# Kernel optimization log

Hardware: AMD Instinct MI355X
Metric: run time of the kernel (lower is better)

## Reference

```python
import jax, jax.numpy as jnp
import numpy as np

EMBED_DIM = 512
NUM_HEADS = 8
HEAD_DIM = EMBED_DIM // NUM_HEADS
PAIR_BONUS = 2.0
MIN_SEPARATION = 3
PAIRING_MATRIX = jnp.array([
    [0, 1, 0, 0, 0],
    [1, 0, 1, 0, 0],
    [0, 1, 0, 1, 0],
    [0, 0, 1, 0, 0],
    [0, 0, 0, 0, 0],
], dtype=jnp.float32)


def setup_inputs() -> dict:
    key = jax.random.key(0)
    ks = jax.random.split(key, 12)
    B, S, E = 8, 1024, EMBED_DIM
    scale = 1.0 / np.sqrt(E)
    inp = {
        "query": jax.random.normal(ks[0], (B, S, E), dtype=jnp.float32),
        "key": jax.random.normal(ks[1], (B, S, E), dtype=jnp.float32),
        "value": jax.random.normal(ks[2], (B, S, E), dtype=jnp.float32),
        "nucleotide_sequence": jax.random.randint(ks[3], (B, S), 0, 5, dtype=jnp.int32),
        "key_padding_mask": jnp.zeros((B, S), dtype=bool),
        "Wq": jax.random.normal(ks[4], (E, E), dtype=jnp.float32) * scale,
        "bq": jnp.zeros((E,), dtype=jnp.float32),
        "Wk": jax.random.normal(ks[5], (E, E), dtype=jnp.float32) * scale,
        "bk": jnp.zeros((E,), dtype=jnp.float32),
        "Wv": jax.random.normal(ks[6], (E, E), dtype=jnp.float32) * scale,
        "bv": jnp.zeros((E,), dtype=jnp.float32),
        "Wo": jax.random.normal(ks[7], (E, E), dtype=jnp.float32) * scale,
        "bo": jnp.zeros((E,), dtype=jnp.float32),
    }
    return inp


def reference(query, key, value, nucleotide_sequence, key_padding_mask,
              Wq, bq, Wk, bk, Wv, bv, Wo, bo):
    B, T, E = query.shape
    S = key.shape[1]
    H, D = NUM_HEADS, HEAD_DIM
    scaling = D ** -0.5

    # projections -> (B, H, L, D)
    q = (query @ Wq + bq).reshape(B, T, H, D).transpose(0, 2, 1, 3)
    k = (key @ Wk + bk).reshape(B, S, H, D).transpose(0, 2, 1, 3)
    v = (value @ Wv + bv).reshape(B, S, H, D).transpose(0, 2, 1, 3)

    attn = jnp.einsum('bhtd,bhsd->bhts', q, k) * scaling  # (B,H,T,S)

    # base-pairing bias: gather into 5x5 table, masked by min separation
    pos = jnp.arange(S)
    sep_ok = (jnp.abs(pos[:, None] - pos[None, :]) >= MIN_SEPARATION).astype(jnp.float32)
    pairing = PAIRING_MATRIX[nucleotide_sequence[:, :, None], nucleotide_sequence[:, None, :]]  # (B,S,S)
    pair_bonus = pairing * sep_ok[None] * PAIR_BONUS
    attn = attn + pair_bonus[:, None, :, :]

    # key padding mask -> -inf
    attn = jnp.where(key_padding_mask[:, None, None, :], -jnp.inf, attn)

    attn_probs = jax.nn.softmax(attn, axis=-1)
    out = jnp.einsum('bhts,bhsd->bhtd', attn_probs, v)
    out = out.transpose(0, 2, 1, 3).reshape(B, T, E)
    out = out @ Wo + bo
    return out, attn_probs
```

## Files before the change

### kernel.cpp

```cpp
#include <hip/hip_runtime.h>
#include <hip/hip_bf16.h>
#include <stdint.h>


typedef float  f32x4  __attribute__((ext_vector_type(4)));
typedef short  s16x8  __attribute__((ext_vector_type(8)));

__device__ __forceinline__ ushort f2bf(float f) {
  union { float f; uint32_t u; } v; v.f = f;
  uint32_t u = v.u;
  return (ushort)((u + 0x7FFF + ((u >> 16) & 1)) >> 16);
}

__device__ __forceinline__ float bf2f(uint32_t u) {
  union { uint32_t u; float f; } v; v.u = u << 16;
  return v.f;
}

__device__ __forceinline__ f32x4 mfma16(s16x8 a, s16x8 b, f32x4 c) {
  return __builtin_amdgcn_mfma_f32_16x16x32_bf16(a, b, c, 0, 0, 0);
}

__device__ __forceinline__ void gl_lds16(const void* g, void* l) {
  typedef __attribute__((address_space(1))) const void gvoid;
  typedef __attribute__((address_space(3))) void lvoid;
  __builtin_amdgcn_global_load_lds((gvoid*)(uintptr_t)g,
                                   (lvoid*)(uint32_t)(uintptr_t)l, 16, 0, 0);
}

__device__ __forceinline__ void vwait4() {
  asm volatile("s_waitcnt vmcnt(4)" ::: "memory");
  __builtin_amdgcn_sched_barrier(0);
}
__device__ __forceinline__ void vwait0() {
  asm volatile("s_waitcnt vmcnt(0)" ::: "memory");
  __builtin_amdgcn_sched_barrier(0);
}
__device__ __forceinline__ void bar_lds() {
  asm volatile("s_waitcnt lgkmcnt(0)" ::: "memory");
  __builtin_amdgcn_s_barrier();
  __builtin_amdgcn_sched_barrier(0);
}

__global__ __launch_bounds__(256) void k_convert_w(
    const float* __restrict__ Wq, const float* __restrict__ Wk,
    const float* __restrict__ Wv, const float* __restrict__ Wo,
    ushort* __restrict__ WT, ushort* __restrict__ WoT) {
  int idx = blockIdx.x * 256 + threadIdx.x;
  int row = idx >> 9;
  int k = idx & 511;
  if (row < 1536) {
    const float* W = (row < 512) ? Wq : (row < 1024 ? Wk : Wv);
    int n = row & 511;
    WT[row * 512 + k] = f2bf(W[k * 512 + n]);
  } else {
    int n = row - 1536;
    WoT[n * 512 + k] = f2bf(Wo[k * 512 + n]);
  }
}

__global__ __launch_bounds__(256) void k_gemm_qkv(
    const float* __restrict__ Aq, const float* __restrict__ Ak,
    const float* __restrict__ Av, const ushort* __restrict__ WT,
    const float* __restrict__ bq, const float* __restrict__ bk,
    const float* __restrict__ bv, ushort* __restrict__ Y) {
  __shared__ ushort As[128 * 64];
  __shared__ ushort Bs[128 * 64];
  const int id = blockIdx.x;
  const int xcd = id & 7, slot = id >> 3;
  const int mb = xcd * 8 + slot / 12;
  const int nb = slot % 12;
  const int mat = nb >> 2;
  const float* A    = (mat == 0) ? Aq : (mat == 1 ? Ak : Av);
  const float* bias = (mat == 0) ? bq : (mat == 1 ? bk : bv);
  const int tid = threadIdx.x;
  const int w = tid >> 6, l = tid & 63;
  const int wr = (w >> 1) * 64, wc = (w & 1) * 64;
  const int lr = l & 15, lg = l >> 4;
  const int srow = l >> 3, sslot = (l & 7) ^ srow;

  f32x4 acc[4][4];
#pragma unroll
  for (int i = 0; i < 4; i++)
#pragma unroll
    for (int j = 0; j < 4; j++) acc[i][j] = (f32x4){0.f, 0.f, 0.f, 0.f};

  for (int kk = 0; kk < 8; kk++) {
    const int k0 = kk * 64;
#pragma unroll
    for (int it = 0; it < 8; it++) {
      int s2 = it * 256 + tid;
      int row = s2 >> 4;
      int k4 = (s2 & 15) * 4;
      float4 v = *reinterpret_cast<const float4*>(
          &A[(size_t)(mb * 128 + row) * 512 + k0 + k4]);
      uint64_t p = (uint64_t)f2bf(v.x) | ((uint64_t)f2bf(v.y) << 16) |
                   ((uint64_t)f2bf(v.z) << 32) | ((uint64_t)f2bf(v.w) << 48);
      int boff = row * 128 + ((k4 * 2) ^ ((row & 7) << 4));
      *reinterpret_cast<uint64_t*>((char*)As + boff) = p;
    }
#pragma unroll
    for (int it = 0; it < 4; it++) {
      int g8 = it * 4 + w;
      int row = g8 * 8 + srow;
      gl_lds16(&WT[(size_t)(nb * 128 + row) * 512 + k0 + sslot * 8], &Bs[g8 * 512]);
    }
    __syncthreads();
#pragma unroll
    for (int ks = 0; ks < 2; ks++) {
      s16x8 af[4], bfr[4];
#pragma unroll
      for (int mt = 0; mt < 4; mt++) {
        int row = wr + mt * 16 + lr;
        af[mt] = *reinterpret_cast<const s16x8*>(
            (char*)As + row * 128 + ((ks * 64 + lg * 16) ^ ((row & 7) << 4)));
      }
#pragma unroll
      for (int nt = 0; nt < 4; nt++) {
        int row = wc + nt * 16 + lr;
        bfr[nt] = *reinterpret_cast<const s16x8*>(
            (char*)Bs + row * 128 + ((ks * 64 + lg * 16) ^ ((row & 7) << 4)));
      }
#pragma unroll
      for (int mt = 0; mt < 4; mt++)
#pragma unroll
        for (int nt = 0; nt < 4; nt++)
          acc[mt][nt] = mfma16(af[mt], bfr[nt], acc[mt][nt]);
    }
    __syncthreads();
  }
  const int ncb = nb * 128;
#pragma unroll
  for (int nt = 0; nt < 4; nt++) {
    int gcol = ncb + wc + nt * 16 + lr;
    float bv_ = bias[gcol & 511];
#pragma unroll
    for (int mt = 0; mt < 4; mt++) {
#pragma unroll
      for (int r = 0; r < 4; r++) {
        int grow = mb * 128 + wr + mt * 16 + lg * 4 + r;
        Y[(size_t)grow * 1536 + gcol] = f2bf(acc[mt][nt][r] + bv_);
      }
    }
  }
}

__global__ __launch_bounds__(256) void k_transpose_v(
    const ushort* __restrict__ Y, ushort* __restrict__ vT) {
  __shared__ ushort T[64 * 64];
  const int sc = blockIdx.x;
  const int bh = blockIdx.y;
  const int b = bh >> 3, h = bh & 7;
  const int s0 = sc * 64;
  const int tid = threadIdx.x;
#pragma unroll
  for (int it = 0; it < 2; it++) {
    int slot = it * 256 + tid;
    int srw = slot >> 3;
    int i16 = (slot & 7) * 16;
    int4 v = *reinterpret_cast<const int4*>(
        &Y[(size_t)(b * 1024 + s0 + srw) * 1536 + 1024 + h * 64 + (slot & 7) * 8]);
    *reinterpret_cast<int4*>((char*)T + srw * 128 + (i16 ^ ((srw & 7) << 4))) = v;
  }
  __syncthreads();
  const int d = tid >> 2;
  const int sseg = (tid & 3) * 16;
  int pk[8];
#pragma unroll
  for (int j = 0; j < 8; j++) {
    int s0l = sseg + 2 * j;
    uint32_t a = *reinterpret_cast<const ushort*>(
        (char*)T + s0l * 128 + ((d * 2) ^ ((s0l & 7) << 4)));
    uint32_t bb = *reinterpret_cast<const ushort*>(
        (char*)T + (s0l + 1) * 128 + ((d * 2) ^ (((s0l + 1) & 7) << 4)));
    pk[j] = (int)(a | (bb << 16));
  }
  ushort* dst = &vT[(size_t)(bh * 64 + d) * 1024 + s0 + sseg];
  int4 o0 = {pk[0], pk[1], pk[2], pk[3]};
  int4 o1 = {pk[4], pk[5], pk[6], pk[7]};
  *reinterpret_cast<int4*>(dst) = o0;
  *reinterpret_cast<int4*>(dst + 8) = o1;
}

__global__ __launch_bounds__(256, 4) void k_attention(
    const ushort* __restrict__ Y, const ushort* __restrict__ vT,
    const int* __restrict__ seq, const unsigned char* __restrict__ mask,
    float* __restrict__ probs, ushort* __restrict__ AO) {
  __shared__ ushort Kb[2][4096];
  __shared__ ushort Vb[2][4096];
  __shared__ ushort Qb[1024];
  __shared__ ushort Pb[16 * 72];
  __shared__ ushort seqm[1024];
  __shared__ float rinv_s[16];
  float* Rbuf = reinterpret_cast<float*>(&Kb[0][0]);

  const int id = blockIdx.x;
  const int xcd = id & 7, slot = id >> 3;
  const int bh = xcd * 8 + (slot >> 6);
  const int tb = slot & 63;
  const int b = bh >> 3, h = bh & 7;
  const int tid = threadIdx.x;
  const int w = tid >> 6, l = tid & 63;
  const int lr = l & 15, lg = l >> 4;
  const int sc_ = w * 16;
  const int srw = sc_ + lr;
  const int srow = l >> 3, sslot = (l & 7) ^ srow;

#pragma unroll
  for (int it = 0; it < 4; it++) {
    int s = it * 256 + tid;
    seqm[s] = (ushort)(seq[b * 1024 + s] | (mask[b * 1024 + s] ? 0x100 : 0));
  }
#pragma unroll
  for (int it = 0; it < 2; it++) {
    int g8 = w * 2 + it;
    int row = g8 * 8 + srow;
    gl_lds16(&Y[(size_t)(b * 1024 + row) * 1536 + 512 + h * 64 + sslot * 8],
             &Kb[0][g8 * 512]);
    gl_lds16(&vT[(size_t)(bh * 64 + row) * 1024 + sslot * 8], &Vb[0][g8 * 512]);
  }
  if (w < 2) {
    gl_lds16(&Y[(size_t)(b * 1024 + tb * 16 + w * 8 + srow) * 1536 + h * 64 +
                sslot * 8],
             &Qb[w * 512]);
  }
  __syncthreads();

  s16x8 qf0 = *reinterpret_cast<const s16x8*>(
      (char*)Qb + lr * 128 + ((lg * 16) ^ ((lr & 7) << 4)));
  s16x8 qf1 = *reinterpret_cast<const s16x8*>(
      (char*)Qb + lr * 128 + ((64 + lg * 16) ^ ((lr & 7) << 4)));
  int seqt[4];
#pragma unroll
  for (int r = 0; r < 4; r++) seqt[r] = seqm[tb * 16 + lg * 4 + r] & 255;

  uint2 pe[16];
  float psum[4] = {0.f, 0.f, 0.f, 0.f};
  f32x4 oacc = (f32x4){0.f, 0.f, 0.f, 0.f};

#pragma unroll
  for (int c = 0; c < 16; c++) {
    if (c < 15) {
#pragma unroll
      for (int it = 0; it < 2; it++) {
        int g8 = w * 2 + it;
        int row = g8 * 8 + srow;
        gl_lds16(&Y[(size_t)(b * 1024 + (c + 1) * 64 + row) * 1536 + 512 +
                    h * 64 + sslot * 8],
                 &Kb[(c + 1) & 1][g8 * 512]);
        gl_lds16(&vT[(size_t)(bh * 64 + row) * 1024 + (c + 1) * 64 + sslot * 8],
                 &Vb[(c + 1) & 1][g8 * 512]);
      }
      vwait4();
    } else {
      vwait0();
    }
    s16x8 kf0 = *reinterpret_cast<const s16x8*>(
        (char*)&Kb[c & 1][0] + srw * 128 + ((lg * 16) ^ ((srw & 7) << 4)));
    s16x8 kf1 = *reinterpret_cast<const s16x8*>(
        (char*)&Kb[c & 1][0] + srw * 128 + ((64 + lg * 16) ^ ((srw & 7) << 4)));
    f32x4 facc = (f32x4){0.f, 0.f, 0.f, 0.f};
    facc = mfma16(qf0, kf0, facc);
    facc = mfma16(qf1, kf1, facc);

    const int sg = c * 64 + srw;
    const int sm = seqm[sg];
    const int ss = sm & 255;
    const bool msk = (sm & 0x100) != 0;
    ushort eb[4];
#pragma unroll
    for (int r = 0; r < 4; r++) {
      int tg = tb * 16 + lg * 4 + r;
      int dsep = tg - sg; dsep = dsep < 0 ? -dsep : dsep;
      int dnt = seqt[r] - ss; dnt = dnt < 0 ? -dnt : dnt;
      bool bon = (dnt == 1 && seqt[r] <= 3 && ss <= 3 && dsep >= 3);
      float v = facc[r] * 0.125f + (bon ? 2.0f : 0.0f);
      float ee = msk ? 0.0f : __expf(v - 12.0f);
      psum[r] += ee;
      eb[r] = f2bf(ee);
      Pb[(lg * 4 + r) * 72 + srw] = eb[r];
    }
    pe[c].x = (uint32_t)eb[0] | ((uint32_t)eb[1] << 16);
    pe[c].y = (uint32_t)eb[2] | ((uint32_t)eb[3] << 16);
    bar_lds();

#pragma unroll
    for (int ks = 0; ks < 2; ks++) {
      s16x8 paf = *reinterpret_cast<const s16x8*>(&Pb[lr * 72 + ks * 32 + lg * 8]);
      s16x8 vb = *reinterpret_cast<const s16x8*>(
          (char*)&Vb[c & 1][0] + srw * 128 +
          ((ks * 64 + lg * 16) ^ ((srw & 7) << 4)));
      oacc = mfma16(paf, vb, oacc);
    }
    bar_lds();
  }

#pragma unroll
  for (int r = 0; r < 4; r++) Rbuf[((w * 4 + lg) * 4 + r) * 16 + lr] = psum[r];
  __syncthreads();
  {
    int row = tid >> 4, j = tid & 15;
    int lgr = row >> 2, rr = row & 3;
    float s = 0.f;
#pragma unroll
    for (int i = 0; i < 4; i++) {
      int wj = j >> 2;
      int lrj = (j & 3) * 4 + i;
      s += Rbuf[((wj * 4 + lgr) * 4 + rr) * 16 + lrj];
    }
#pragma unroll
    for (int off = 1; off < 16; off <<= 1) s += __shfl_xor(s, off);
    if (j == 0) rinv_s[row] = 1.0f / s;
  }
  __syncthreads();
  float rv[4];
#pragma unroll
  for (int r = 0; r < 4; r++) rv[r] = rinv_s[lg * 4 + r];

#pragma unroll
  for (int r = 0; r < 4; r++) {
    int t = tb * 16 + lg * 4 + r;
    AO[((size_t)b * 1024 + t) * 512 + h * 64 + sc_ + lr] = f2bf(oacc[r] * rv[r]);
  }

  float* Pf = reinterpret_cast<float*>(&Kb[0][0]);
  const int prow_ = tid >> 4, pj = tid & 15;
  float* pdst_base = &probs[((size_t)bh * 1024 + tb * 16 + prow_) * 1024 + pj * 4];
#pragma unroll
  for (int c = 0; c < 16; c++) {
#pragma unroll
    for (int r = 0; r < 4; r++) {
      uint32_t u = (r < 2) ? pe[c].x : pe[c].y;
      u = (u >> ((r & 1) * 16)) & 0xffffu;
      Pf[(lg * 4 + r) * 68 + srw] = bf2f(u) * rv[r];
    }
    bar_lds();
    float4 p4 = *reinterpret_cast<const float4*>(&Pf[prow_ * 68 + pj * 4]);
    *reinterpret_cast<float4*>(pdst_base + c * 64) = p4;
    bar_lds();
  }
}

__global__ __launch_bounds__(256) void k_gemm_o(
    const ushort* __restrict__ AO, const ushort* __restrict__ WoT,
    const float* __restrict__ bo, float* __restrict__ out) {
  __shared__ ushort As[128 * 64];
  __shared__ ushort Bs[128 * 64];
  const int id = blockIdx.x;
  const int xcd = id & 7, slot = id >> 3;
  const int mb = xcd * 8 + (slot >> 2);
  const int nb = slot & 3;
  const int tid = threadIdx.x;
  const int w = tid >> 6, l = tid & 63;
  const int wr = (w >> 1) * 64, wc = (w & 1) * 64;
  const int lr = l & 15, lg = l >> 4;
  const int srow = l >> 3, sslot = (l & 7) ^ srow;

  f32x4 acc[4][4];
#pragma unroll
  for (int i = 0; i < 4; i++)
#pragma unroll
    for (int j = 0; j < 4; j++) acc[i][j] = (f32x4){0.f, 0.f, 0.f, 0.f};

  for (int kk = 0; kk < 8; kk++) {
    const int k0 = kk * 64;
#pragma unroll
    for (int it = 0; it < 4; it++) {
      int g8 = it * 4 + w;
      int row = g8 * 8 + srow;
      gl_lds16(&AO[(size_t)(mb * 128 + row) * 512 + k0 + sslot * 8], &As[g8 * 512]);
      gl_lds16(&WoT[(size_t)(nb * 128 + row) * 512 + k0 + sslot * 8], &Bs[g8 * 512]);
    }
    __syncthreads();
#pragma unroll
    for (int ks = 0; ks < 2; ks++) {
      s16x8 af[4], bfr[4];
#pragma unroll
      for (int mt = 0; mt < 4; mt++) {
        int row = wr + mt * 16 + lr;
        af[mt] = *reinterpret_cast<const s16x8*>(
            (char*)As + row * 128 + ((ks * 64 + lg * 16) ^ ((row & 7) << 4)));
      }
#pragma unroll
      for (int nt = 0; nt < 4; nt++) {
        int row = wc + nt * 16 + lr;
        bfr[nt] = *reinterpret_cast<const s16x8*>(
            (char*)Bs + row * 128 + ((ks * 64 + lg * 16) ^ ((row & 7) << 4)));
      }
#pragma unroll
      for (int mt = 0; mt < 4; mt++)
#pragma unroll
        for (int nt = 0; nt < 4; nt++)
          acc[mt][nt] = mfma16(af[mt], bfr[nt], acc[mt][nt]);
    }
    __syncthreads();
  }
  const int ncb = nb * 128;
#pragma unroll
  for (int nt = 0; nt < 4; nt++) {
    int gcol = ncb + wc + nt * 16 + lr;
    float bv_ = bo[gcol];
#pragma unroll
    for (int mt = 0; mt < 4; mt++) {
#pragma unroll
      for (int r = 0; r < 4; r++) {
        int grow = mb * 128 + wr + mt * 16 + lg * 4 + r;
        out[(size_t)grow * 512 + gcol] = acc[mt][nt][r] + bv_;
      }
    }
  }
}

extern "C" void kernel_launch(void* const* d_in, const int* in_sizes, int n_in,
                              void* d_out, int out_size, void* d_ws, size_t ws_size,
                              hipStream_t stream) {
  (void)in_sizes; (void)n_in; (void)out_size; (void)ws_size;
  const float* query = (const float*)d_in[0];
  const float* key   = (const float*)d_in[1];
  const float* value = (const float*)d_in[2];
  const int* seq     = (const int*)d_in[3];
  const unsigned char* mask = (const unsigned char*)d_in[4];
  const float* Wq = (const float*)d_in[5];
  const float* bq = (const float*)d_in[6];
  const float* Wk = (const float*)d_in[7];
  const float* bk = (const float*)d_in[8];
  const float* Wv = (const float*)d_in[9];
  const float* bv = (const float*)d_in[10];
  const float* Wo = (const float*)d_in[11];
  const float* bo = (const float*)d_in[12];

  float* out = (float*)d_out;
  float* probs = out + (size_t)8 * 1024 * 512;

  char* ws = (char*)d_ws;
  ushort* Y   = (ushort*)(ws);
  ushort* WT  = (ushort*)(ws + 25165824);
  ushort* WoT = (ushort*)(ws + 26738688);
  ushort* vT  = (ushort*)(ws + 27262976);
  ushort* AO  = (ushort*)(ws + 35651584);

  k_convert_w<<<4096, 256, 0, stream>>>(Wq, Wk, Wv, Wo, WT, WoT);
  k_gemm_qkv<<<768, 256, 0, stream>>>(query, key, value, WT, bq, bk, bv, Y);
  k_transpose_v<<<dim3(16, 64), 256, 0, stream>>>(Y, vT);
  k_attention<<<4096, 256, 0, stream>>>(Y, vT, seq, mask, probs, AO);
  k_gemm_o<<<256, 256, 0, stream>>>(AO, WoT, bo, out);
}
```

Baseline: 217.1 us.

## Split probability output into separate kernel that recomputes QK scores

```diff
diff --git a/kernel.cpp b/kernel.cpp
--- a/kernel.cpp
+++ b/kernel.cpp
@@ -10,11 +10,6 @@
   union { float f; uint32_t u; } v; v.f = f;
   uint32_t u = v.u;
   return (ushort)((u + 0x7FFF + ((u >> 16) & 1)) >> 16);
-}
-
-__device__ __forceinline__ float bf2f(uint32_t u) {
-  union { uint32_t u; float f; } v; v.u = u << 16;
-  return v.f;
 }
 
 __device__ __forceinline__ f32x4 mfma16(s16x8 a, s16x8 b, f32x4 c) {
@@ -30,6 +25,10 @@
 
 __device__ __forceinline__ void vwait4() {
   asm volatile("s_waitcnt vmcnt(4)" ::: "memory");
+  __builtin_amdgcn_sched_barrier(0);
+}
+__device__ __forceinline__ void vwait2() {
+  asm volatile("s_waitcnt vmcnt(2)" ::: "memory");
   __builtin_amdgcn_sched_barrier(0);
 }
 __device__ __forceinline__ void vwait0() {
@@ -182,10 +181,10 @@
   *reinterpret_cast<int4*>(dst + 8) = o1;
 }
 
-__global__ __launch_bounds__(256, 4) void k_attention(
+__global__ __launch_bounds__(256, 4) void k_attn_core(
     const ushort* __restrict__ Y, const ushort* __restrict__ vT,
     const int* __restrict__ seq, const unsigned char* __restrict__ mask,
-    float* __restrict__ probs, ushort* __restrict__ AO) {
+    float* __restrict__ rinv_ws, ushort* __restrict__ AO) {
   __shared__ ushort Kb[2][4096];
   __shared__ ushort Vb[2][4096];
   __shared__ ushort Qb[1024];
@@ -234,7 +233,6 @@
 #pragma unroll
   for (int r = 0; r < 4; r++) seqt[r] = seqm[tb * 16 + lg * 4 + r] & 255;
 
-  uint2 pe[16];
   float psum[4] = {0.f, 0.f, 0.f, 0.f};
   f32x4 oacc = (f32x4){0.f, 0.f, 0.f, 0.f};
 
@@ -267,7 +265,6 @@
     const int sm = seqm[sg];
     const int ss = sm & 255;
     const bool msk = (sm & 0x100) != 0;
-    ushort eb[4];
 #pragma unroll
     for (int r = 0; r < 4; r++) {
       int tg = tb * 16 + lg * 4 + r;
@@ -277,11 +274,8 @@
       float v = facc[r] * 0.125f + (bon ? 2.0f : 0.0f);
       float ee = msk ? 0.0f : __expf(v - 12.0f);
       psum[r] += ee;
-      eb[r] = f2bf(ee);
-      Pb[(lg * 4 + r) * 72 + srw] = eb[r];
-    }
-    pe[c].x = (uint32_t)eb[0] | ((uint32_t)eb[1] << 16);
-    pe[c].y = (uint32_t)eb[2] | ((uint32_t)eb[3] << 16);
+      Pb[(lg * 4 + r) * 72 + srw] = f2bf(ee);
+    }
     bar_lds();
 
 #pragma unroll
@@ -313,6 +307,8 @@
     if (j == 0) rinv_s[row] = 1.0f / s;
   }
   __syncthreads();
+  if (tid < 16)
+    rinv_ws[(size_t)bh * 1024 + tb * 16 + tid] = rinv_s[tid];
   float rv[4];
 #pragma unroll
   for (int r = 0; r < 4; r++) rv[r] = rinv_s[lg * 4 + r];
@@ -322,22 +318,99 @@
     int t = tb * 16 + lg * 4 + r;
     AO[((size_t)b * 1024 + t) * 512 + h * 64 + sc_ + lr] = f2bf(oacc[r] * rv[r]);
   }
-
-  float* Pf = reinterpret_cast<float*>(&Kb[0][0]);
-  const int prow_ = tid >> 4, pj = tid & 15;
-  float* pdst_base = &probs[((size_t)bh * 1024 + tb * 16 + prow_) * 1024 + pj * 4];
+}
+
+__global__ __launch_bounds__(256, 8) void k_probs(
+    const ushort* __restrict__ Y, const float* __restrict__ rinv_ws,
+    const int* __restrict__ seq, const unsigned char* __restrict__ mask,
+    float* __restrict__ probs) {
+  __shared__ ushort Kb[2][4096];
+  __shared__ ushort Qb[1024];
+  __shared__ unsigned char seqm8[1024];
+
+  const int id = blockIdx.x;
+  const int xcd = id & 7, slot = id >> 3;
+  const int bh = xcd * 8 + (slot >> 6);
+  const int tb = slot & 63;
+  const int b = bh >> 3, h = bh & 7;
+  const int tid = threadIdx.x;
+  const int w = tid >> 6, l = tid & 63;
+  const int lr = l & 15, lg = l >> 4;
+  const int srw = w * 16 + lr;
+  const int srow = l >> 3, sslot = (l & 7) ^ srow;
+
+#pragma unroll
+  for (int it = 0; it < 4; it++) {
+    int s = it * 256 + tid;
+    seqm8[s] =
+        (unsigned char)(seq[b * 1024 + s] | (mask[b * 1024 + s] ? 16 : 0));
+  }
+#pragma unroll
+  for (int it = 0; it < 2; it++) {
+    int g8 = w * 2 + it;
+    int row = g8 * 8 + srow;
+    gl_lds16(&Y[(size_t)(b * 1024 + row) * 1536 + 512 + h * 64 + sslot * 8],
+             &Kb[0][g8 * 512]);
+  }
+  if (w < 2) {
+    gl_lds16(&Y[(size_t)(b * 1024 + tb * 16 + w * 8 + srow) * 1536 + h * 64 +
+                sslot * 8],
+             &Qb[w * 512]);
+  }
+  __syncthreads();
+
+  s16x8 qf0 = *reinterpret_cast<const s16x8*>(
+      (char*)Qb + lr * 128 + ((lg * 16) ^ ((lr & 7) << 4)));
+  s16x8 qf1 = *reinterpret_cast<const s16x8*>(
+      (char*)Qb + lr * 128 + ((64 + lg * 16) ^ ((lr & 7) << 4)));
+  int seqt[4];
+  float rv[4];
+  float* prow[4];
+#pragma unroll
+  for (int r = 0; r < 4; r++) {
+    int t = tb * 16 + lg * 4 + r;
+    seqt[r] = seqm8[t] & 15;
+    rv[r] = rinv_ws[(size_t)bh * 1024 + t];
+    prow[r] = &probs[((size_t)bh * 1024 + t) * 1024 + srw];
+  }
+
 #pragma unroll
   for (int c = 0; c < 16; c++) {
+    if (c < 15) {
+#pragma unroll
+      for (int it = 0; it < 2; it++) {
+        int g8 = w * 2 + it;
+        int row = g8 * 8 + srow;
+        gl_lds16(&Y[(size_t)(b * 1024 + (c + 1) * 64 + row) * 1536 + 512 +
+                    h * 64 + sslot * 8],
+                 &Kb[(c + 1) & 1][g8 * 512]);
+      }
+      vwait2();
+    } else {
+      vwait0();
+    }
+    s16x8 kf0 = *reinterpret_cast<const s16x8*>(
+        (char*)&Kb[c & 1][0] + srw * 128 + ((lg * 16) ^ ((srw & 7) << 4)));
+    s16x8 kf1 = *reinterpret_cast<const s16x8*>(
+        (char*)&Kb[c & 1][0] + srw * 128 + ((64 + lg * 16) ^ ((srw & 7) << 4)));
+    f32x4 facc = (f32x4){0.f, 0.f, 0.f, 0.f};
+    facc = mfma16(qf0, kf0, facc);
+    facc = mfma16(qf1, kf1, facc);
+
+    const int sg = c * 64 + srw;
+    const int sm = seqm8[sg];
+    const int ss = sm & 15;
+    const bool msk = (sm & 16) != 0;
 #pragma unroll
     for (int r = 0; r < 4; r++) {
-      uint32_t u = (r < 2) ? pe[c].x : pe[c].y;
-      u = (u >> ((r & 1) * 16)) & 0xffffu;
-      Pf[(lg * 4 + r) * 68 + srw] = bf2f(u) * rv[r];
-    }
-    bar_lds();
-    float4 p4 = *reinterpret_cast<const float4*>(&Pf[prow_ * 68 + pj * 4]);
-    *reinterpret_cast<float4*>(pdst_base + c * 64) = p4;
-    bar_lds();
+      int tg = tb * 16 + lg * 4 + r;
+      int dsep = tg - sg; dsep = dsep < 0 ? -dsep : dsep;
+      int dnt = seqt[r] - ss; dnt = dnt < 0 ? -dnt : dnt;
+      bool bon = (dnt == 1 && seqt[r] <= 3 && ss <= 3 && dsep >= 3);
+      float v = facc[r] * 0.125f + (bon ? 2.0f : 0.0f);
+      float ee = msk ? 0.0f : __expf(v - 12.0f);
+      __builtin_nontemporal_store(ee * rv[r], prow[r] + c * 64);
+    }
   }
 }
 
@@ -433,15 +506,17 @@
   float* probs = out + (size_t)8 * 1024 * 512;
 
   char* ws = (char*)d_ws;
-  ushort* Y   = (ushort*)(ws);
-  ushort* WT  = (ushort*)(ws + 25165824);
-  ushort* WoT = (ushort*)(ws + 26738688);
-  ushort* vT  = (ushort*)(ws + 27262976);
-  ushort* AO  = (ushort*)(ws + 35651584);
+  ushort* Y      = (ushort*)(ws);
+  ushort* WT     = (ushort*)(ws + 25165824);
+  ushort* WoT    = (ushort*)(ws + 26738688);
+  ushort* vT     = (ushort*)(ws + 27262976);
+  ushort* AO     = (ushort*)(ws + 35651584);
+  float*  rinv_ws= (float*)(ws + 44040192);
 
   k_convert_w<<<4096, 256, 0, stream>>>(Wq, Wk, Wv, Wo, WT, WoT);
   k_gemm_qkv<<<768, 256, 0, stream>>>(query, key, value, WT, bq, bk, bv, Y);
   k_transpose_v<<<dim3(16, 64), 256, 0, stream>>>(Y, vT);
-  k_attention<<<4096, 256, 0, stream>>>(Y, vT, seq, mask, probs, AO);
+  k_attn_core<<<4096, 256, 0, stream>>>(Y, vT, seq, mask, rinv_ws, AO);
+  k_probs<<<4096, 256, 0, stream>>>(Y, rinv_ws, seq, mask, probs);
   k_gemm_o<<<256, 256, 0, stream>>>(AO, WoT, bo, out);
 }
```

Result: slower. 226.8 us (+4.5%).
